# Kernel tuning notes

Hardware: AMD Instinct MI355X
Metric: run time of the kernel (lower is better)

The kernel has to match this reference:

```python
import jax, jax.numpy as jnp
import numpy as np

DIM = 1024
HEADS = 16
HEAD_DIM = DIM // HEADS
SCALE = HEAD_DIM ** -0.5


def apply_rope(x, theta=10000.0):
    # x: [b, h, n, d]
    n, d = x.shape[2], x.shape[3]
    seq = jnp.arange(n, dtype=jnp.float32)
    inv = 1.0 / (theta ** (jnp.arange(0, d, 2, dtype=jnp.float32) / d))  # [d/2]
    freqs = seq[:, None] * inv[None, :]  # [n, d/2]
    cos = jnp.cos(freqs)[None, None]  # [1,1,n,d/2]
    sin = jnp.sin(freqs)[None, None]
    x1, x2 = jnp.split(x, 2, axis=-1)
    return jnp.concatenate([x1 * cos - x2 * sin, x1 * sin + x2 * cos], axis=-1)


def setup_inputs() -> dict:
    key = jax.random.key(0)
    ks = jax.random.split(key, 7)
    s = DIM ** -0.5
    return {
        "x": jax.random.normal(ks[0], (2, 2048, DIM), dtype=jnp.float32),
        "Wqkv": jax.random.normal(ks[1], (3 * DIM, DIM), dtype=jnp.float32) * s,
        "bqkv": jax.random.normal(ks[2], (3 * DIM,), dtype=jnp.float32) * 0.02,
        "Wpre": jax.random.normal(ks[3], (HEADS, HEADS), dtype=jnp.float32) * HEADS ** -0.5,
        "Wpost": jax.random.normal(ks[4], (HEADS, HEADS), dtype=jnp.float32) * HEADS ** -0.5,
        "Wout": jax.random.normal(ks[5], (DIM, DIM), dtype=jnp.float32) * s,
        "bout": jax.random.normal(ks[6], (DIM,), dtype=jnp.float32) * 0.02,
    }


def reference(x, Wqkv, bqkv, Wpre, Wpost, Wout, bout):
    b, n, _ = x.shape
    qkv = x @ Wqkv.T + bqkv  # [b, n, 3*dim]
    q, k, v = jnp.split(qkv, 3, axis=-1)
    # [b, n, dim] -> [b, h, n, d]
    reshape = lambda t: t.reshape(b, n, HEADS, HEAD_DIM).transpose(0, 2, 1, 3)
    q, k, v = reshape(q), reshape(k), reshape(v)
    q = apply_rope(q)
    k = apply_rope(k)
    logits = jnp.einsum('bhid,bhjd->bhij', q, k) * SCALE
    # pre-softmax talking heads: Linear(heads->heads), y[...,g] = sum_h x[...,h] * Wpre[g,h]
    logits = jnp.einsum('bhij,gh->bgij', logits, Wpre)
    attn = jax.nn.softmax(logits, axis=-1)
    attn = jnp.einsum('bhij,gh->bgij', attn, Wpost)
    out = jnp.einsum('bhij,bhjd->bhid', attn, v)
    out = out.transpose(0, 2, 1, 3).reshape(b, n, DIM)
    return out @ Wout.T + bout
```

## Files before the change

### kernel.cpp

```cpp
#include <hip/hip_runtime.h>
#include <cstddef>
#include <cstdint>

#define SEQ    2048
#define DMODEL 1024
#define NHEAD  16
#define HDIM   64
#define SCALE  0.125f
#define LOG2E  1.4426950408889634f

typedef _Float16 f16;
typedef unsigned short u16;
typedef unsigned int   u32;
typedef __attribute__((ext_vector_type(8))) _Float16 h8v;
typedef __attribute__((ext_vector_type(4))) _Float16 h4v;
typedef __attribute__((ext_vector_type(4))) float    f4v;

__device__ __forceinline__ u32 pkh(float a, float b) {
    u16 x = __builtin_bit_cast(u16, (f16)a);
    u16 y = __builtin_bit_cast(u16, (f16)b);
    return (u32)x | ((u32)y << 16);
}

__device__ __forceinline__ float fexp2(float x) {
#if __has_builtin(__builtin_amdgcn_exp2f)
    return __builtin_amdgcn_exp2f(x);
#else
    return exp2f(x);
#endif
}

__device__ __forceinline__ f4v mfma32(h8v a, h8v b, f4v c) {
    return __builtin_amdgcn_mfma_f32_16x16x32_f16(a, b, c, 0, 0, 0);
}
__device__ __forceinline__ f4v mfma16(h4v a, h4v b, f4v c) {
    return __builtin_amdgcn_mfma_f32_16x16x16f16(a, b, c, 0, 0, 0);
}

__global__ __launch_bounds__(256)
void cvt_f16_kernel(const float* __restrict__ x, const float* __restrict__ Wqkv,
                    const float* __restrict__ Wout,
                    f16* __restrict__ Xh, f16* __restrict__ Wqh, f16* __restrict__ Woh)
{
    size_t i = ((size_t)blockIdx.x * 256 + threadIdx.x) * 8;
    const float* src; f16* dst; size_t off;
    if (i < 4194304)      { src = x;    dst = Xh;  off = i; }
    else if (i < 7340032) { src = Wqkv; dst = Wqh; off = i - 4194304; }
    else                  { src = Wout; dst = Woh; off = i - 7340032; }
    float4 a = *(const float4*)&src[off];
    float4 b = *(const float4*)&src[off + 4];
    uint4 o;
    o.x = pkh(a.x, a.y); o.y = pkh(a.z, a.w);
    o.z = pkh(b.x, b.y); o.w = pkh(b.z, b.w);
    *(uint4*)&dst[off] = o;
}

__global__ __launch_bounds__(256)
void gemm_f16_kernel(const f16* __restrict__ A, const f16* __restrict__ B,
                     const float* __restrict__ bias, void* __restrict__ Cout,
                     int N, int K, int mode)
{
    __shared__ __align__(16) char Asb[8192];
    __shared__ __align__(16) char Bsb[8192];
    int tid = threadIdx.x;
    int w = tid >> 6, l = tid & 63, lr = l & 15, lc = l >> 4;
    int row0 = blockIdx.y * 128, col0 = blockIdx.x * 128;
    int wr = (w >> 1) * 64, wc = (w & 1) * 64;

    f4v acc[4][4];
    #pragma unroll
    for (int m = 0; m < 4; ++m)
        #pragma unroll
        for (int n = 0; n < 4; ++n) acc[m][n] = (f4v){0.f, 0.f, 0.f, 0.f};

    int r0 = tid >> 2, k0s = tid & 3;
    int r1 = (tid + 256) >> 2, k1s = tid & 3;

    uint4 ra0, ra1, rb0, rb1;
    ra0 = *(const uint4*)&A[(size_t)(row0 + r0) * K + k0s * 8];
    ra1 = *(const uint4*)&A[(size_t)(row0 + r1) * K + k1s * 8];
    rb0 = *(const uint4*)&B[(size_t)(col0 + r0) * K + k0s * 8];
    rb1 = *(const uint4*)&B[(size_t)(col0 + r1) * K + k1s * 8];

    int NT = K >> 5;
    for (int kt = 0; kt < NT; ++kt) {
        *(uint4*)(Asb + r0 * 64 + ((k0s ^ (r0 & 3)) << 4)) = ra0;
        *(uint4*)(Asb + r1 * 64 + ((k1s ^ (r1 & 3)) << 4)) = ra1;
        *(uint4*)(Bsb + r0 * 64 + ((k0s ^ (r0 & 3)) << 4)) = rb0;
        *(uint4*)(Bsb + r1 * 64 + ((k1s ^ (r1 & 3)) << 4)) = rb1;
        if (kt + 1 < NT) {
            int kk = (kt + 1) * 32;
            ra0 = *(const uint4*)&A[(size_t)(row0 + r0) * K + kk + k0s * 8];
            ra1 = *(const uint4*)&A[(size_t)(row0 + r1) * K + kk + k1s * 8];
            rb0 = *(const uint4*)&B[(size_t)(col0 + r0) * K + kk + k0s * 8];
            rb1 = *(const uint4*)&B[(size_t)(col0 + r1) * K + kk + k1s * 8];
        }
        __syncthreads();
        h8v af[4], bf[4];
        #pragma unroll
        for (int m = 0; m < 4; ++m) {
            int row = wr + m * 16 + lr;
            af[m] = *(h8v*)(Asb + row * 64 + ((lc ^ (row & 3)) << 4));
        }
        #pragma unroll
        for (int n = 0; n < 4; ++n) {
            int col = wc + n * 16 + lr;
            bf[n] = *(h8v*)(Bsb + col * 64 + ((lc ^ (col & 3)) << 4));
        }
        #pragma unroll
        for (int m = 0; m < 4; ++m)
            #pragma unroll
            for (int n = 0; n < 4; ++n)
                acc[m][n] = mfma32(af[m], bf[n], acc[m][n]);
        __syncthreads();
    }

    #pragma unroll
    for (int m = 0; m < 4; ++m)
        #pragma unroll
        for (int r = 0; r < 4; ++r) {
            int row = row0 + wr + m * 16 + lc * 4 + r;
            #pragma unroll
            for (int n = 0; n < 4; ++n) {
                int col = col0 + wc + n * 16 + lr;
                float v = acc[m][n][r] + bias[col];
                if (mode == 0) ((f16*)Cout)[(size_t)row * N + col] = (f16)v;
                else           ((float*)Cout)[(size_t)row * N + col] = v;
            }
        }
}

__global__ __launch_bounds__(256)
void pack_qk_kernel(const f16* __restrict__ QKVh, f16* __restrict__ Qh, f16* __restrict__ Kh)
{
    int gid = blockIdx.x * 256 + threadIdx.x;
    int i     = gid & 15;
    int t8    = (gid >> 4) & 3;
    int h     = (gid >> 6) & 15;
    int rh    = (gid >> 10) & 255;
    int which = (gid >> 18) & 1;
    int row = rh * 16 + i;
    int pos = row & (SEQ - 1);
    int b   = row >> 11;
    f16* dst = which ? Kh : Qh;

    h8v x1 = *(const h8v*)&QKVh[(size_t)row * 3072 + which * 1024 + h * 64 + t8 * 8];
    h8v x2 = *(const h8v*)&QKVh[(size_t)row * 3072 + which * 1024 + h * 64 + t8 * 8 + 32];

    float y1[8], y2[8];
    #pragma unroll
    for (int e = 0; e < 8; ++e) {
        int t = t8 * 8 + e;
        float inv = exp2f((float)(-2 * t) * (0.015625f * 13.287712379549449f));
        float ang = (float)pos * inv;
        float c, s;
        sincosf(ang, &s, &c);
        float a1 = (float)x1[e], a2 = (float)x2[e];
        y1[e] = a1 * c - a2 * s;
        y2[e] = a1 * s + a2 * c;
    }
    int it = pos >> 4;
    size_t b0 = (((((size_t)(b*128 + it)*16 + h)*2 + 0)*4 + t8)*16 + i)*8;
    size_t b1 = (((((size_t)(b*128 + it)*16 + h)*2 + 1)*4 + t8)*16 + i)*8;
    uint4 o0, o1;
    o0.x = pkh(y1[0], y1[1]); o0.y = pkh(y1[2], y1[3]);
    o0.z = pkh(y1[4], y1[5]); o0.w = pkh(y1[6], y1[7]);
    o1.x = pkh(y2[0], y2[1]); o1.y = pkh(y2[2], y2[3]);
    o1.z = pkh(y2[4], y2[5]); o1.w = pkh(y2[6], y2[7]);
    *(uint4*)(dst + b0) = o0;
    *(uint4*)(dst + b1) = o1;
}

__global__ __launch_bounds__(256)
void pack_v_kernel(const f16* __restrict__ QKVh, f16* __restrict__ Vt)
{
    int gid = blockIdx.x * 256 + threadIdx.x;
    int dd = gid & 15;
    int jc = (gid >> 4) & 3;
    int dt = (gid >> 6) & 3;
    int g  = (gid >> 8) & 15;
    int jt = (gid >> 12) & 63;
    int b  = (gid >> 18) & 1;
    int d = g * 64 + dt * 16 + dd;
    f16 v[8];
    #pragma unroll
    for (int e = 0; e < 8; ++e) {
        int j = jt * 32 + jc * 8 + e;
        v[e] = QKVh[(size_t)(b * SEQ + j) * 3072 + 2048 + d];
    }
    size_t off = ((((((size_t)b*64 + jt)*16 + g)*4 + dt)*4 + jc)*16 + dd)*8;
    uint4 o;
    o.x = pkh((float)v[0], (float)v[1]); o.y = pkh((float)v[2], (float)v[3]);
    o.z = pkh((float)v[4], (float)v[5]); o.w = pkh((float)v[6], (float)v[7]);
    *(uint4*)(Vt + off) = o;
}

__global__ __launch_bounds__(256)
void pack_ctx_kernel(const f16* __restrict__ Cp, f16* __restrict__ Ch)
{
    size_t i = ((size_t)blockIdx.x * 256 + threadIdx.x) * 8;
    h8v p0 = *(const h8v*)&Cp[i];
    h8v p1 = *(const h8v*)&Cp[i + 4194304];
    h8v p2 = *(const h8v*)&Cp[i + 8388608];
    h8v p3 = *(const h8v*)&Cp[i + 12582912];
    float s[8];
    #pragma unroll
    for (int e = 0; e < 8; ++e)
        s[e] = (float)p0[e] + (float)p1[e] + (float)p2[e] + (float)p3[e];
    uint4 o;
    o.x = pkh(s[0], s[1]); o.y = pkh(s[2], s[3]);
    o.z = pkh(s[4], s[5]); o.w = pkh(s[6], s[7]);
    *(uint4*)&Ch[i] = o;
}

template<int FULL>
__global__ __launch_bounds__(512, 2)
void attn_core(const f16* __restrict__ Qh, const f16* __restrict__ Kh,
               const f16* __restrict__ Vt, const float* __restrict__ Wpre,
               const float* __restrict__ Wpost, const float* __restrict__ Zp,
               float* __restrict__ Zout, f16* __restrict__ Octx)
{
    __shared__ __align__(16) char ss[2 * 16384];
    __shared__ __align__(16) char es[FULL ? 2 * 16384 : 16];
    __shared__ float zred[FULL ? 512 : 4096];

    int tid = threadIdx.x;
    int wv = tid >> 6;
    int l  = tid & 63;
    int lr = l & 15;
    int lc = l >> 4;

    int bid   = blockIdx.x;
    int it2   = bid & 63;
    int b     = (bid >> 6) & 1;
    int split = bid >> 7;

    h4v wpre4;
    #pragma unroll
    for (int e = 0; e < 4; ++e) wpre4[e] = (f16)(Wpre[lr * 16 + lc * 4 + e] * (SCALE * LOG2E));
    h4v wpost;
    if (FULL) {
        #pragma unroll
        for (int e = 0; e < 4; ++e) wpost[e] = (f16)Wpost[lr * 16 + lc * 4 + e];
    }

    h8v qf[2][2][2];
    #pragma unroll
    for (int itl = 0; itl < 2; ++itl)
        #pragma unroll
        for (int hh = 0; hh < 2; ++hh)
            #pragma unroll
            for (int ks = 0; ks < 2; ++ks) {
                size_t off = ((((size_t)((b*128 + it2*2 + itl)*16 + (wv*2 + hh))*2 + ks)*4 + lc)*16 + lr)*8;
                qf[itl][hh][ks] = *(const h8v*)(Qh + off);
            }

    float m4[2][4];
    float zacc[2][4] = {};
    if (FULL) {
        int itl = tid >> 8, g = (tid >> 4) & 15, i = tid & 15;
        size_t idx = (size_t)(b * 16 + g) * SEQ + it2 * 32 + itl * 16 + i;
        zred[tid] = log2f(Zp[idx] + Zp[65536 + idx] + Zp[131072 + idx] + Zp[196608 + idx]);
        __syncthreads();
        #pragma unroll
        for (int itl2 = 0; itl2 < 2; ++itl2)
            #pragma unroll
            for (int r = 0; r < 4; ++r)
                m4[itl2][r] = zred[itl2 * 256 + (lc * 4 + r) * 16 + lr];
    }

    f4v pv[2][2][4];
    if (FULL) {
        #pragma unroll
        for (int itl = 0; itl < 2; ++itl)
            #pragma unroll
            for (int gg = 0; gg < 2; ++gg)
                #pragma unroll
                for (int dt = 0; dt < 4; ++dt) pv[itl][gg][dt] = (f4v){0.f, 0.f, 0.f, 0.f};
    }

    int j0beg = split * 512;
    int jtbeg = j0beg >> 4;

    h8v kfA[2][2][2], kfB[2][2][2];
    #pragma unroll
    for (int hh = 0; hh < 2; ++hh)
        #pragma unroll
        for (int js = 0; js < 2; ++js)
            #pragma unroll
            for (int ks = 0; ks < 2; ++ks) {
                size_t off = ((((size_t)((b*128 + jtbeg + js)*16 + (wv*2 + hh))*2 + ks)*4 + lc)*16 + lr)*8;
                kfA[hh][js][ks] = *(const h8v*)(Kh + off);
            }

    auto step = [&](int s, h8v (&kfU)[2][2][2], h8v (&kfP)[2][2][2]) {
        int j0 = j0beg + s * 32;
        h8v vf[2][4];
        if (FULL) {
            #pragma unroll
            for (int gg = 0; gg < 2; ++gg)
                #pragma unroll
                for (int dt = 0; dt < 4; ++dt) {
                    size_t voff = (((((size_t)(b*64 + (j0 >> 5))*16 + (wv*2 + gg))*4 + dt)*4 + lc)*16 + lr)*8;
                    vf[gg][dt] = *(const h8v*)(Vt + voff);
                }
        }
        f4v qk[2][2][2];
        __builtin_amdgcn_s_setprio(1);
        #pragma unroll
        for (int itl = 0; itl < 2; ++itl)
            #pragma unroll
            for (int hh = 0; hh < 2; ++hh)
                #pragma unroll
                for (int js = 0; js < 2; ++js) {
                    f4v a = (f4v){0.f, 0.f, 0.f, 0.f};
                    a = mfma32(qf[itl][hh][0], kfU[hh][js][0], a);
                    a = mfma32(qf[itl][hh][1], kfU[hh][js][1], a);
                    qk[itl][hh][js] = a;
                }
        __builtin_amdgcn_s_setprio(0);
        {
            int sp = (s + 1 < 16) ? (s + 1) : 0;
            int jt0 = jtbeg + sp * 2;
            #pragma unroll
            for (int hh = 0; hh < 2; ++hh)
                #pragma unroll
                for (int js = 0; js < 2; ++js)
                    #pragma unroll
                    for (int ks = 0; ks < 2; ++ks) {
                        size_t off = ((((size_t)((b*128 + jt0 + js)*16 + (wv*2 + hh))*2 + ks)*4 + lc)*16 + lr)*8;
                        kfP[hh][js][ks] = *(const h8v*)(Kh + off);
                    }
        }
        #pragma unroll
        for (int itl = 0; itl < 2; ++itl)
            #pragma unroll
            for (int js = 0; js < 2; ++js)
                #pragma unroll
                for (int r = 0; r < 4; ++r) {
                    int i = lc * 4 + r;
                    int addr = itl * 16384 + ((wv >> 1) * 2 + js) * 2048 + i * 128
                             + ((lr ^ i) << 3) + (wv & 1) * 4;
                    *(u32*)(ss + addr) = pkh(qk[itl][0][js][r], qk[itl][1][js][r]);
                }
        __syncthreads();

        u32 a2p[2][4][2];
        #pragma unroll
        for (int itl = 0; itl < 2; ++itl)
            #pragma unroll
            for (int tt = 0; tt < 4; ++tt) {
                int t = wv * 4 + tt;
                int addr = itl * 16384 + (lc * 2 + (t >> 4)) * 2048 + lr * 128
                         + (((t & 15) ^ lr) << 3);
                union { uint2 u; h4v v; } cv;
                cv.u = *(uint2*)(ss + addr);
                f4v s1 = mfma16(wpre4, cv.v, (f4v){0.f, 0.f, 0.f, 0.f});
                if (!FULL) {
                    #pragma unroll
                    for (int r = 0; r < 4; ++r) zacc[itl][r] += fexp2(s1[r]);
                } else {
                    h4v pf;
                    #pragma unroll
                    for (int r = 0; r < 4; ++r) pf[r] = (f16)fexp2(s1[r] - m4[itl][r]);
                    f4v a2 = mfma16(wpost, pf, (f4v){0.f, 0.f, 0.f, 0.f});
                    #pragma unroll
                    for (int r = 0; r < 4; ++r) {
                        u32 v = (u32)__builtin_bit_cast(u16, (f16)a2[r]);
                        if (tt & 1) a2p[itl][r][tt >> 1] |= v << 16;
                        else        a2p[itl][r][tt >> 1]  = v;
                    }
                }
            }
        if (FULL) {
            #pragma unroll
            for (int itl = 0; itl < 2; ++itl)
                #pragma unroll
                for (int r = 0; r < 4; ++r) {
                    int gq = lc * 4 + r;
                    int off = itl * 16384 + ((gq * 1024 + lr * 64 + wv * 8) ^ ((lr & 7) << 4));
                    *(uint2*)(es + off) = make_uint2(a2p[itl][r][0], a2p[itl][r][1]);
                }
        }
        __syncthreads();

        if (FULL) {
            __builtin_amdgcn_s_setprio(1);
            #pragma unroll
            for (int gg = 0; gg < 2; ++gg) {
                int g = wv * 2 + gg;
                #pragma unroll
                for (int itl = 0; itl < 2; ++itl) {
                    h8v af = *(h8v*)(es + itl * 16384
                                     + ((g * 1024 + lr * 64 + lc * 16) ^ ((lr & 7) << 4)));
                    #pragma unroll
                    for (int dt = 0; dt < 4; ++dt)
                        pv[itl][gg][dt] = mfma32(af, vf[gg][dt], pv[itl][gg][dt]);
                }
            }
            __builtin_amdgcn_s_setprio(0);
        }
    };

    for (int s = 0; s < 16; s += 2) {
        step(s,     kfA, kfB);
        step(s + 1, kfB, kfA);
    }

    if (!FULL) {
        #pragma unroll
        for (int itl = 0; itl < 2; ++itl)
            #pragma unroll
            for (int r = 0; r < 4; ++r)
                zred[itl * 2048 + ((lc * 4 + r) * 16 + lr) * 8 + wv] = zacc[itl][r];
        __syncthreads();
        int itl = tid >> 8, gi = tid & 255;
        float z = 0.f;
        #pragma unroll
        for (int w2 = 0; w2 < 8; ++w2) z += zred[itl * 2048 + gi * 8 + w2];
        int g = gi >> 4, i = gi & 15;
        Zout[(size_t)split * 65536 + (size_t)(b * 16 + g) * SEQ + it2 * 32 + itl * 16 + i] = z;
    } else {
        f16* dst = Octx + (size_t)split * 4194304;
        #pragma unroll
        for (int itl = 0; itl < 2; ++itl)
            #pragma unroll
            for (int gg = 0; gg < 2; ++gg)
                #pragma unroll
                for (int dt = 0; dt < 4; ++dt)
                    #pragma unroll
                    for (int r = 0; r < 4; ++r) {
                        int row = it2 * 32 + itl * 16 + lc * 4 + r;
                        int col = (wv * 2 + gg) * 64 + dt * 16 + lr;
                        dst[(size_t)(b * SEQ + row) * DMODEL + col] = (f16)pv[itl][gg][dt][r];
                    }
    }
}

extern "C" void kernel_launch(void* const* d_in, const int* in_sizes, int n_in,
                              void* d_out, int out_size, void* d_ws, size_t ws_size,
                              hipStream_t stream)
{
    const float* x     = (const float*)d_in[0];
    const float* Wqkv  = (const float*)d_in[1];
    const float* bqkv  = (const float*)d_in[2];
    const float* Wpre  = (const float*)d_in[3];
    const float* Wpost = (const float*)d_in[4];
    const float* Wout  = (const float*)d_in[5];
    const float* bout  = (const float*)d_in[6];
    float* out = (float*)d_out;

    float* ws = (float*)d_ws;
    f16*   QKVh = (f16*)(ws);
    f16*   CTXp = (f16*)(ws);
    f16*   Xh   = (f16*)(ws + 8388608);
    f16*   Wqh  = (f16*)(ws + 10485760);
    f16*   Woh  = (f16*)(ws + 12058624);
    f16*   Qh   = (f16*)(ws + 12582912);
    f16*   Kh   = (f16*)(ws + 14680064);
    f16*   Vt   = (f16*)(ws + 16777216);
    f16*   Ch   = (f16*)(ws + 18874368);
    float* Zp   = ws + 19922944;

    dim3 blk(256);
    cvt_f16_kernel<<<4096, blk, 0, stream>>>(x, Wqkv, Wout, Xh, Wqh, Woh);
    gemm_f16_kernel<<<dim3(24, 32), blk, 0, stream>>>(Xh, Wqh, bqkv, (void*)QKVh, 3072, 1024, 0);
    pack_qk_kernel<<<2048, blk, 0, stream>>>(QKVh, Qh, Kh);
    pack_v_kernel<<<2048, blk, 0, stream>>>(QKVh, Vt);
    attn_core<0><<<512, dim3(512), 0, stream>>>(Qh, Kh, Vt, Wpre, Wpost, nullptr, Zp, nullptr);
    attn_core<1><<<512, dim3(512), 0, stream>>>(Qh, Kh, Vt, Wpre, Wpost, Zp, nullptr, CTXp);
    pack_ctx_kernel<<<2048, blk, 0, stream>>>(CTXp, Ch);
    gemm_f16_kernel<<<dim3(8, 32), blk, 0, stream>>>(Ch, Woh, bout, (void*)out, 1024, 1024, 1);
}
```

Before: 215.9 us.

## Software-pipeline attention steps with double-buffered LDS and one barrier per step

Restructures the attention inner loop so each iteration mixes heads and applies softmax for tile s, computes QK^T for tile s+1 into the other LDS buffer, and runs the PV MFMAs for tile s-1 from the previous buffer. This cuts the barriers per step from two to one and lets MFMA work from different stages overlap. The LDS score and probability buffers are doubled to make this possible, which raises shared memory per block and may reduce the number of resident blocks per CU.

```diff
diff --git a/kernel.cpp b/kernel.cpp
--- a/kernel.cpp
+++ b/kernel.cpp
@@ -220,8 +220,8 @@
                const float* __restrict__ Wpost, const float* __restrict__ Zp,
                float* __restrict__ Zout, f16* __restrict__ Octx)
 {
-    __shared__ __align__(16) char ss[2 * 16384];
-    __shared__ __align__(16) char es[FULL ? 2 * 16384 : 16];
+    __shared__ __align__(16) char ss[2 * 32768];
+    __shared__ __align__(16) char es[FULL ? 2 * 32768 : 16];
     __shared__ float zred[FULL ? 512 : 4096];
 
     int tid = threadIdx.x;
@@ -255,104 +255,101 @@
                 qf[itl][hh][ks] = *(const h8v*)(Qh + off);
             }
 
+    if (FULL) {
+        int g = (tid >> 4) & 15, i = tid & 15, itl = tid >> 8;
+        size_t idx = (size_t)(b * 16 + g) * SEQ + it2 * 32 + itl * 16 + i;
+        zred[tid] = log2f(Zp[idx] + Zp[65536 + idx] + Zp[131072 + idx] + Zp[196608 + idx]);
+    }
+
+    f4v pv[2][2][4];
+    if (FULL) {
+        #pragma unroll
+        for (int itl = 0; itl < 2; ++itl)
+            #pragma unroll
+            for (int gg = 0; gg < 2; ++gg)
+                #pragma unroll
+                for (int dt = 0; dt < 4; ++dt) pv[itl][gg][dt] = (f4v){0.f, 0.f, 0.f, 0.f};
+    }
+
+    int j0beg = split * 512;
+    int jtbeg = j0beg >> 4;
+
+    auto ldK = [&](int s, h8v (&kf)[2][2][2]) {
+        int jt0 = jtbeg + s * 2;
+        #pragma unroll
+        for (int hh = 0; hh < 2; ++hh)
+            #pragma unroll
+            for (int js = 0; js < 2; ++js)
+                #pragma unroll
+                for (int ks = 0; ks < 2; ++ks) {
+                    size_t off = ((((size_t)((b*128 + jt0 + js)*16 + (wv*2 + hh))*2 + ks)*4 + lc)*16 + lr)*8;
+                    kf[hh][js][ks] = *(const h8v*)(Kh + off);
+                }
+    };
+    auto ldV = [&](int s, h8v (&vf)[2][4]) {
+        int jt32 = (j0beg >> 5) + s;
+        #pragma unroll
+        for (int gg = 0; gg < 2; ++gg)
+            #pragma unroll
+            for (int dt = 0; dt < 4; ++dt) {
+                size_t voff = (((((size_t)(b*64 + jt32)*16 + (wv*2 + gg))*4 + dt)*4 + lc)*16 + lr)*8;
+                vf[gg][dt] = *(const h8v*)(Vt + voff);
+            }
+    };
+    auto qkt = [&](const h8v (&kf)[2][2][2], int pb) {
+        #pragma unroll
+        for (int itl = 0; itl < 2; ++itl)
+            #pragma unroll
+            for (int js = 0; js < 2; ++js) {
+                f4v q0 = (f4v){0.f, 0.f, 0.f, 0.f};
+                q0 = mfma32(qf[itl][0][0], kf[0][js][0], q0);
+                q0 = mfma32(qf[itl][0][1], kf[0][js][1], q0);
+                f4v q1 = (f4v){0.f, 0.f, 0.f, 0.f};
+                q1 = mfma32(qf[itl][1][0], kf[1][js][0], q1);
+                q1 = mfma32(qf[itl][1][1], kf[1][js][1], q1);
+                #pragma unroll
+                for (int r = 0; r < 4; ++r) {
+                    int i = lc * 4 + r;
+                    int addr = pb * 32768 + itl * 16384 + ((wv >> 1) * 2 + js) * 2048
+                             + i * 128 + ((lr ^ i) << 3) + (wv & 1) * 4;
+                    *(u32*)(ss + addr) = pkh(q0[r], q1[r]);
+                }
+            }
+    };
+
+    {
+        h8v kf0[2][2][2];
+        ldK(0, kf0);
+        qkt(kf0, 0);
+    }
+    __syncthreads();
+
     float m4[2][4];
     float zacc[2][4] = {};
     if (FULL) {
-        int itl = tid >> 8, g = (tid >> 4) & 15, i = tid & 15;
-        size_t idx = (size_t)(b * 16 + g) * SEQ + it2 * 32 + itl * 16 + i;
-        zred[tid] = log2f(Zp[idx] + Zp[65536 + idx] + Zp[131072 + idx] + Zp[196608 + idx]);
-        __syncthreads();
-        #pragma unroll
-        for (int itl2 = 0; itl2 < 2; ++itl2)
+        #pragma unroll
+        for (int itl = 0; itl < 2; ++itl)
             #pragma unroll
             for (int r = 0; r < 4; ++r)
-                m4[itl2][r] = zred[itl2 * 256 + (lc * 4 + r) * 16 + lr];
-    }
-
-    f4v pv[2][2][4];
-    if (FULL) {
-        #pragma unroll
-        for (int itl = 0; itl < 2; ++itl)
-            #pragma unroll
-            for (int gg = 0; gg < 2; ++gg)
-                #pragma unroll
-                for (int dt = 0; dt < 4; ++dt) pv[itl][gg][dt] = (f4v){0.f, 0.f, 0.f, 0.f};
-    }
-
-    int j0beg = split * 512;
-    int jtbeg = j0beg >> 4;
-
-    h8v kfA[2][2][2], kfB[2][2][2];
-    #pragma unroll
-    for (int hh = 0; hh < 2; ++hh)
-        #pragma unroll
-        for (int js = 0; js < 2; ++js)
-            #pragma unroll
-            for (int ks = 0; ks < 2; ++ks) {
-                size_t off = ((((size_t)((b*128 + jtbeg + js)*16 + (wv*2 + hh))*2 + ks)*4 + lc)*16 + lr)*8;
-                kfA[hh][js][ks] = *(const h8v*)(Kh + off);
-            }
-
-    auto step = [&](int s, h8v (&kfU)[2][2][2], h8v (&kfP)[2][2][2]) {
-        int j0 = j0beg + s * 32;
+                m4[itl][r] = zred[itl * 256 + (lc * 4 + r) * 16 + lr];
+    }
+
+    for (int s = 0; s < 16; ++s) {
+        int pb = s & 1, pn = pb ^ 1;
+
         h8v vf[2][4];
-        if (FULL) {
-            #pragma unroll
-            for (int gg = 0; gg < 2; ++gg)
-                #pragma unroll
-                for (int dt = 0; dt < 4; ++dt) {
-                    size_t voff = (((((size_t)(b*64 + (j0 >> 5))*16 + (wv*2 + gg))*4 + dt)*4 + lc)*16 + lr)*8;
-                    vf[gg][dt] = *(const h8v*)(Vt + voff);
-                }
-        }
-        f4v qk[2][2][2];
-        __builtin_amdgcn_s_setprio(1);
-        #pragma unroll
-        for (int itl = 0; itl < 2; ++itl)
-            #pragma unroll
-            for (int hh = 0; hh < 2; ++hh)
-                #pragma unroll
-                for (int js = 0; js < 2; ++js) {
-                    f4v a = (f4v){0.f, 0.f, 0.f, 0.f};
-                    a = mfma32(qf[itl][hh][0], kfU[hh][js][0], a);
-                    a = mfma32(qf[itl][hh][1], kfU[hh][js][1], a);
-                    qk[itl][hh][js] = a;
-                }
-        __builtin_amdgcn_s_setprio(0);
-        {
-            int sp = (s + 1 < 16) ? (s + 1) : 0;
-            int jt0 = jtbeg + sp * 2;
-            #pragma unroll
-            for (int hh = 0; hh < 2; ++hh)
-                #pragma unroll
-                for (int js = 0; js < 2; ++js)
-                    #pragma unroll
-                    for (int ks = 0; ks < 2; ++ks) {
-                        size_t off = ((((size_t)((b*128 + jt0 + js)*16 + (wv*2 + hh))*2 + ks)*4 + lc)*16 + lr)*8;
-                        kfP[hh][js][ks] = *(const h8v*)(Kh + off);
-                    }
-        }
-        #pragma unroll
-        for (int itl = 0; itl < 2; ++itl)
-            #pragma unroll
-            for (int js = 0; js < 2; ++js)
-                #pragma unroll
-                for (int r = 0; r < 4; ++r) {
-                    int i = lc * 4 + r;
-                    int addr = itl * 16384 + ((wv >> 1) * 2 + js) * 2048 + i * 128
-                             + ((lr ^ i) << 3) + (wv & 1) * 4;
-                    *(u32*)(ss + addr) = pkh(qk[itl][0][js][r], qk[itl][1][js][r]);
-                }
-        __syncthreads();
-
-        u32 a2p[2][4][2];
-        #pragma unroll
-        for (int itl = 0; itl < 2; ++itl)
+        if (FULL && s >= 1) ldV(s - 1, vf);
+        h8v kf[2][2][2];
+        if (s < 15) ldK(s + 1, kf);
+
+        #pragma unroll
+        for (int itl = 0; itl < 2; ++itl) {
+            u32 a2p[4][2];
             #pragma unroll
             for (int tt = 0; tt < 4; ++tt) {
                 int t = wv * 4 + tt;
-                int addr = itl * 16384 + (lc * 2 + (t >> 4)) * 2048 + lr * 128
-                         + (((t & 15) ^ lr) << 3);
+                int addr = pb * 32768 + itl * 16384 + (lc * 2 + (t >> 4)) * 2048
+                         + lr * 128 + (((t & 15) ^ lr) << 3);
                 union { uint2 u; h4v v; } cv;
                 cv.u = *(uint2*)(ss + addr);
                 f4v s1 = mfma16(wpre4, cv.v, (f4v){0.f, 0.f, 0.f, 0.f});
@@ -367,44 +364,56 @@
                     #pragma unroll
                     for (int r = 0; r < 4; ++r) {
                         u32 v = (u32)__builtin_bit_cast(u16, (f16)a2[r]);
-                        if (tt & 1) a2p[itl][r][tt >> 1] |= v << 16;
-                        else        a2p[itl][r][tt >> 1]  = v;
+                        if (tt & 1) a2p[r][tt >> 1] |= v << 16;
+                        else        a2p[r][tt >> 1]  = v;
                     }
                 }
             }
-        if (FULL) {
-            #pragma unroll
-            for (int itl = 0; itl < 2; ++itl)
+            if (FULL) {
                 #pragma unroll
                 for (int r = 0; r < 4; ++r) {
                     int gq = lc * 4 + r;
-                    int off = itl * 16384 + ((gq * 1024 + lr * 64 + wv * 8) ^ ((lr & 7) << 4));
-                    *(uint2*)(es + off) = make_uint2(a2p[itl][r][0], a2p[itl][r][1]);
+                    int off = pb * 32768 + itl * 16384
+                            + ((gq * 1024 + lr * 64 + wv * 8) ^ ((lr & 7) << 4));
+                    *(uint2*)(es + off) = make_uint2(a2p[r][0], a2p[r][1]);
                 }
-        }
-        __syncthreads();
-
-        if (FULL) {
-            __builtin_amdgcn_s_setprio(1);
+            }
+        }
+
+        if (s < 15) qkt(kf, pn);
+
+        if (FULL && s >= 1) {
             #pragma unroll
             for (int gg = 0; gg < 2; ++gg) {
                 int g = wv * 2 + gg;
                 #pragma unroll
                 for (int itl = 0; itl < 2; ++itl) {
-                    h8v af = *(h8v*)(es + itl * 16384
+                    h8v af = *(h8v*)(es + pn * 32768 + itl * 16384
                                      + ((g * 1024 + lr * 64 + lc * 16) ^ ((lr & 7) << 4)));
                     #pragma unroll
                     for (int dt = 0; dt < 4; ++dt)
                         pv[itl][gg][dt] = mfma32(af, vf[gg][dt], pv[itl][gg][dt]);
                 }
             }
-            __builtin_amdgcn_s_setprio(0);
-        }
-    };
-
-    for (int s = 0; s < 16; s += 2) {
-        step(s,     kfA, kfB);
-        step(s + 1, kfB, kfA);
+        }
+        __syncthreads();
+    }
+
+    if (FULL) {
+        h8v vf[2][4];
+        ldV(15, vf);
+        #pragma unroll
+        for (int gg = 0; gg < 2; ++gg) {
+            int g = wv * 2 + gg;
+            #pragma unroll
+            for (int itl = 0; itl < 2; ++itl) {
+                h8v af = *(h8v*)(es + 32768 + itl * 16384
+                                 + ((g * 1024 + lr * 64 + lc * 16) ^ ((lr & 7) << 4)));
+                #pragma unroll
+                for (int dt = 0; dt < 4; ++dt)
+                    pv[itl][gg][dt] = mfma32(af, vf[gg][dt], pv[itl][gg][dt]);
+            }
+        }
     }
 
     if (!FULL) {
```

Result: no change. 217.4 us (+0.7%).

## Use 1024-thread attention blocks with one head per wave, drop K prefetch

Applied to the files above, without the earlier changes.

The attention kernels now launch 1024 threads per block, so each of 16 waves handles a single head instead of two. Per-wave register state (Q, K, V fragments and PV accumulators) is halved, and the software double-buffered K prefetch and s_setprio hints are removed in favour of a simple loop. This trades explicit load/compute overlap for more waves in flight, but it narrows the LDS writes to 16-bit stores and makes block-wide barriers span twice as many waves.

```diff
diff --git a/kernel.cpp b/kernel.cpp
--- a/kernel.cpp
+++ b/kernel.cpp
@@ -214,15 +214,15 @@
 }
 
 template<int FULL>
-__global__ __launch_bounds__(512, 2)
+__global__ __launch_bounds__(1024, 1)
 void attn_core(const f16* __restrict__ Qh, const f16* __restrict__ Kh,
                const f16* __restrict__ Vt, const float* __restrict__ Wpre,
                const float* __restrict__ Wpost, const float* __restrict__ Zp,
                float* __restrict__ Zout, f16* __restrict__ Octx)
 {
-    __shared__ __align__(16) char ss[2 * 16384];
-    __shared__ __align__(16) char es[FULL ? 2 * 16384 : 16];
-    __shared__ float zred[FULL ? 512 : 4096];
+    __shared__ __align__(16) char ss[32768];
+    __shared__ __align__(16) char es[FULL ? 32768 : 16];
+    __shared__ float zred[FULL ? 512 : 8192];
 
     int tid = threadIdx.x;
     int wv = tid >> 6;
@@ -244,115 +244,87 @@
         for (int e = 0; e < 4; ++e) wpost[e] = (f16)Wpost[lr * 16 + lc * 4 + e];
     }
 
-    h8v qf[2][2][2];
+    h8v qf[2][2];
     #pragma unroll
     for (int itl = 0; itl < 2; ++itl)
         #pragma unroll
-        for (int hh = 0; hh < 2; ++hh)
-            #pragma unroll
-            for (int ks = 0; ks < 2; ++ks) {
-                size_t off = ((((size_t)((b*128 + it2*2 + itl)*16 + (wv*2 + hh))*2 + ks)*4 + lc)*16 + lr)*8;
-                qf[itl][hh][ks] = *(const h8v*)(Qh + off);
-            }
-
-    float m4[2][4];
-    float zacc[2][4] = {};
-    if (FULL) {
+        for (int ks = 0; ks < 2; ++ks) {
+            size_t off = ((((size_t)((b*128 + it2*2 + itl)*16 + wv)*2 + ks)*4 + lc)*16 + lr)*8;
+            qf[itl][ks] = *(const h8v*)(Qh + off);
+        }
+
+    if (FULL && tid < 512) {
         int itl = tid >> 8, g = (tid >> 4) & 15, i = tid & 15;
         size_t idx = (size_t)(b * 16 + g) * SEQ + it2 * 32 + itl * 16 + i;
         zred[tid] = log2f(Zp[idx] + Zp[65536 + idx] + Zp[131072 + idx] + Zp[196608 + idx]);
-        __syncthreads();
-        #pragma unroll
-        for (int itl2 = 0; itl2 < 2; ++itl2)
+    }
+    __syncthreads();
+
+    float m4[2][4];
+    if (FULL) {
+        #pragma unroll
+        for (int itl = 0; itl < 2; ++itl)
             #pragma unroll
             for (int r = 0; r < 4; ++r)
-                m4[itl2][r] = zred[itl2 * 256 + (lc * 4 + r) * 16 + lr];
-    }
-
-    f4v pv[2][2][4];
+                m4[itl][r] = zred[itl * 256 + (lc * 4 + r) * 16 + lr];
+    }
+
+    f4v pv[2][4];
     if (FULL) {
         #pragma unroll
         for (int itl = 0; itl < 2; ++itl)
             #pragma unroll
-            for (int gg = 0; gg < 2; ++gg)
-                #pragma unroll
-                for (int dt = 0; dt < 4; ++dt) pv[itl][gg][dt] = (f4v){0.f, 0.f, 0.f, 0.f};
-    }
+            for (int dt = 0; dt < 4; ++dt) pv[itl][dt] = (f4v){0.f, 0.f, 0.f, 0.f};
+    }
+    float zacc[2][4] = {};
 
     int j0beg = split * 512;
     int jtbeg = j0beg >> 4;
 
-    h8v kfA[2][2][2], kfB[2][2][2];
-    #pragma unroll
-    for (int hh = 0; hh < 2; ++hh)
+    for (int s = 0; s < 16; ++s) {
+        h8v kf[2][2];
         #pragma unroll
         for (int js = 0; js < 2; ++js)
             #pragma unroll
             for (int ks = 0; ks < 2; ++ks) {
-                size_t off = ((((size_t)((b*128 + jtbeg + js)*16 + (wv*2 + hh))*2 + ks)*4 + lc)*16 + lr)*8;
-                kfA[hh][js][ks] = *(const h8v*)(Kh + off);
-            }
-
-    auto step = [&](int s, h8v (&kfU)[2][2][2], h8v (&kfP)[2][2][2]) {
-        int j0 = j0beg + s * 32;
-        h8v vf[2][4];
+                size_t off = ((((size_t)((b*128 + jtbeg + s*2 + js)*16 + wv)*2 + ks)*4 + lc)*16 + lr)*8;
+                kf[js][ks] = *(const h8v*)(Kh + off);
+            }
+        h8v vf[4];
         if (FULL) {
-            #pragma unroll
-            for (int gg = 0; gg < 2; ++gg)
-                #pragma unroll
-                for (int dt = 0; dt < 4; ++dt) {
-                    size_t voff = (((((size_t)(b*64 + (j0 >> 5))*16 + (wv*2 + gg))*4 + dt)*4 + lc)*16 + lr)*8;
-                    vf[gg][dt] = *(const h8v*)(Vt + voff);
-                }
-        }
-        f4v qk[2][2][2];
-        __builtin_amdgcn_s_setprio(1);
+            int jt32 = (j0beg >> 5) + s;
+            #pragma unroll
+            for (int dt = 0; dt < 4; ++dt) {
+                size_t voff = (((((size_t)(b*64 + jt32)*16 + wv)*4 + dt)*4 + lc)*16 + lr)*8;
+                vf[dt] = *(const h8v*)(Vt + voff);
+            }
+        }
+
         #pragma unroll
         for (int itl = 0; itl < 2; ++itl)
             #pragma unroll
-            for (int hh = 0; hh < 2; ++hh)
-                #pragma unroll
-                for (int js = 0; js < 2; ++js) {
-                    f4v a = (f4v){0.f, 0.f, 0.f, 0.f};
-                    a = mfma32(qf[itl][hh][0], kfU[hh][js][0], a);
-                    a = mfma32(qf[itl][hh][1], kfU[hh][js][1], a);
-                    qk[itl][hh][js] = a;
-                }
-        __builtin_amdgcn_s_setprio(0);
-        {
-            int sp = (s + 1 < 16) ? (s + 1) : 0;
-            int jt0 = jtbeg + sp * 2;
-            #pragma unroll
-            for (int hh = 0; hh < 2; ++hh)
-                #pragma unroll
-                for (int js = 0; js < 2; ++js)
-                    #pragma unroll
-                    for (int ks = 0; ks < 2; ++ks) {
-                        size_t off = ((((size_t)((b*128 + jt0 + js)*16 + (wv*2 + hh))*2 + ks)*4 + lc)*16 + lr)*8;
-                        kfP[hh][js][ks] = *(const h8v*)(Kh + off);
-                    }
-        }
-        #pragma unroll
-        for (int itl = 0; itl < 2; ++itl)
-            #pragma unroll
-            for (int js = 0; js < 2; ++js)
+            for (int js = 0; js < 2; ++js) {
+                f4v q = (f4v){0.f, 0.f, 0.f, 0.f};
+                q = mfma32(qf[itl][0], kf[js][0], q);
+                q = mfma32(qf[itl][1], kf[js][1], q);
                 #pragma unroll
                 for (int r = 0; r < 4; ++r) {
                     int i = lc * 4 + r;
-                    int addr = itl * 16384 + ((wv >> 1) * 2 + js) * 2048 + i * 128
-                             + ((lr ^ i) << 3) + (wv & 1) * 4;
-                    *(u32*)(ss + addr) = pkh(qk[itl][0][js][r], qk[itl][1][js][r]);
+                    int addr = itl * 16384 + ((wv >> 2) * 2 + js) * 2048
+                             + i * 128 + ((lr ^ i) << 3) + (wv & 3) * 2;
+                    *(u16*)(ss + addr) = __builtin_bit_cast(u16, (f16)q[r]);
                 }
+            }
         __syncthreads();
 
-        u32 a2p[2][4][2];
-        #pragma unroll
-        for (int itl = 0; itl < 2; ++itl)
-            #pragma unroll
-            for (int tt = 0; tt < 4; ++tt) {
-                int t = wv * 4 + tt;
-                int addr = itl * 16384 + (lc * 2 + (t >> 4)) * 2048 + lr * 128
-                         + (((t & 15) ^ lr) << 3);
+        #pragma unroll
+        for (int itl = 0; itl < 2; ++itl) {
+            u32 a2p[4];
+            #pragma unroll
+            for (int tt = 0; tt < 2; ++tt) {
+                int t = wv * 2 + tt;
+                int addr = itl * 16384 + (lc * 2 + (t >> 4)) * 2048
+                         + lr * 128 + (((t & 15) ^ lr) << 3);
                 union { uint2 u; h4v v; } cv;
                 cv.u = *(uint2*)(ss + addr);
                 f4v s1 = mfma16(wpre4, cv.v, (f4v){0.f, 0.f, 0.f, 0.f});
@@ -367,44 +339,32 @@
                     #pragma unroll
                     for (int r = 0; r < 4; ++r) {
                         u32 v = (u32)__builtin_bit_cast(u16, (f16)a2[r]);
-                        if (tt & 1) a2p[itl][r][tt >> 1] |= v << 16;
-                        else        a2p[itl][r][tt >> 1]  = v;
+                        if (tt) a2p[r] |= v << 16;
+                        else    a2p[r]  = v;
                     }
                 }
             }
-        if (FULL) {
-            #pragma unroll
-            for (int itl = 0; itl < 2; ++itl)
+            if (FULL) {
                 #pragma unroll
                 for (int r = 0; r < 4; ++r) {
                     int gq = lc * 4 + r;
-                    int off = itl * 16384 + ((gq * 1024 + lr * 64 + wv * 8) ^ ((lr & 7) << 4));
-                    *(uint2*)(es + off) = make_uint2(a2p[itl][r][0], a2p[itl][r][1]);
+                    int off = itl * 16384 + ((gq * 1024 + lr * 64 + wv * 4) ^ ((lr & 7) << 4));
+                    *(u32*)(es + off) = a2p[r];
                 }
+            }
         }
         __syncthreads();
 
         if (FULL) {
-            __builtin_amdgcn_s_setprio(1);
-            #pragma unroll
-            for (int gg = 0; gg < 2; ++gg) {
-                int g = wv * 2 + gg;
+            #pragma unroll
+            for (int itl = 0; itl < 2; ++itl) {
+                h8v af = *(h8v*)(es + itl * 16384
+                                 + ((wv * 1024 + lr * 64 + lc * 16) ^ ((lr & 7) << 4)));
                 #pragma unroll
-                for (int itl = 0; itl < 2; ++itl) {
-                    h8v af = *(h8v*)(es + itl * 16384
-                                     + ((g * 1024 + lr * 64 + lc * 16) ^ ((lr & 7) << 4)));
-                    #pragma unroll
-                    for (int dt = 0; dt < 4; ++dt)
-                        pv[itl][gg][dt] = mfma32(af, vf[gg][dt], pv[itl][gg][dt]);
-                }
-            }
-            __builtin_amdgcn_s_setprio(0);
-        }
-    };
-
-    for (int s = 0; s < 16; s += 2) {
-        step(s,     kfA, kfB);
-        step(s + 1, kfB, kfA);
+                for (int dt = 0; dt < 4; ++dt)
+                    pv[itl][dt] = mfma32(af, vf[dt], pv[itl][dt]);
+            }
+        }
     }
 
     if (!FULL) {
@@ -412,28 +372,28 @@
         for (int itl = 0; itl < 2; ++itl)
             #pragma unroll
             for (int r = 0; r < 4; ++r)
-                zred[itl * 2048 + ((lc * 4 + r) * 16 + lr) * 8 + wv] = zacc[itl][r];
+                zred[itl * 4096 + ((lc * 4 + r) * 16 + lr) * 16 + wv] = zacc[itl][r];
         __syncthreads();
-        int itl = tid >> 8, gi = tid & 255;
-        float z = 0.f;
-        #pragma unroll
-        for (int w2 = 0; w2 < 8; ++w2) z += zred[itl * 2048 + gi * 8 + w2];
-        int g = gi >> 4, i = gi & 15;
-        Zout[(size_t)split * 65536 + (size_t)(b * 16 + g) * SEQ + it2 * 32 + itl * 16 + i] = z;
+        if (tid < 512) {
+            int itl = tid >> 8, gi = tid & 255;
+            float z = 0.f;
+            #pragma unroll
+            for (int w2 = 0; w2 < 16; ++w2) z += zred[itl * 4096 + gi * 16 + w2];
+            int g = gi >> 4, i = gi & 15;
+            Zout[(size_t)split * 65536 + (size_t)(b * 16 + g) * SEQ + it2 * 32 + itl * 16 + i] = z;
+        }
     } else {
         f16* dst = Octx + (size_t)split * 4194304;
         #pragma unroll
         for (int itl = 0; itl < 2; ++itl)
             #pragma unroll
-            for (int gg = 0; gg < 2; ++gg)
+            for (int dt = 0; dt < 4; ++dt)
                 #pragma unroll
-                for (int dt = 0; dt < 4; ++dt)
-                    #pragma unroll
-                    for (int r = 0; r < 4; ++r) {
-                        int row = it2 * 32 + itl * 16 + lc * 4 + r;
-                        int col = (wv * 2 + gg) * 64 + dt * 16 + lr;
-                        dst[(size_t)(b * SEQ + row) * DMODEL + col] = (f16)pv[itl][gg][dt][r];
-                    }
+                for (int r = 0; r < 4; ++r) {
+                    int row = it2 * 32 + itl * 16 + lc * 4 + r;
+                    int col = wv * 64 + dt * 16 + lr;
+                    dst[(size_t)(b * SEQ + row) * DMODEL + col] = (f16)pv[itl][dt][r];
+                }
     }
 }
 
@@ -467,8 +427,8 @@
     gemm_f16_kernel<<<dim3(24, 32), blk, 0, stream>>>(Xh, Wqh, bqkv, (void*)QKVh, 3072, 1024, 0);
     pack_qk_kernel<<<2048, blk, 0, stream>>>(QKVh, Qh, Kh);
     pack_v_kernel<<<2048, blk, 0, stream>>>(QKVh, Vt);
-    attn_core<0><<<512, dim3(512), 0, stream>>>(Qh, Kh, Vt, Wpre, Wpost, nullptr, Zp, nullptr);
-    attn_core<1><<<512, dim3(512), 0, stream>>>(Qh, Kh, Vt, Wpre, Wpost, Zp, nullptr, CTXp);
+    attn_core<0><<<512, dim3(1024), 0, stream>>>(Qh, Kh, Vt, Wpre, Wpost, nullptr, Zp, nullptr);
+    attn_core<1><<<512, dim3(1024), 0, stream>>>(Qh, Kh, Vt, Wpre, Wpost, Zp, nullptr, CTXp);
     pack_ctx_kernel<<<2048, blk, 0, stream>>>(CTXp, Ch);
     gemm_f16_kernel<<<dim3(8, 32), blk, 0, stream>>>(Ch, Woh, bout, (void*)out, 1024, 1024, 1);
 }
```

Result: slower. 220.9 us (+2.3%).
